# Kernel tuning notes

Hardware: AMD Instinct MI355X
Metric: run time of the kernel (lower is better)

Reference implementation:

```python
import jax, jax.numpy as jnp
import numpy as np

GAMMA = 0.9
TEMPERATURE = 0.07
BASE_TEMPERATURE = 0.07
U_SIZE = 15_000_000
BSZ, N_VIEWS, DIM = 2048, 2, 256


def setup_inputs() -> dict:
    key = jax.random.key(0)
    kf, = jax.random.split(key, 1)
    feats = jax.random.normal(kf, (BSZ, N_VIEWS, DIM), dtype=jnp.float32)
    # contrastive features are unit-normalized in practice
    feats = feats / jnp.linalg.norm(feats, axis=-1, keepdims=True)
    index = jnp.arange(BSZ, dtype=jnp.int64) if jax.config.jax_enable_x64 else jnp.arange(BSZ, dtype=jnp.int32)
    u = jnp.zeros((U_SIZE, 1), dtype=jnp.float32)
    return {"index": index, "features": feats, "u": u}


def reference(index, features, u):
    B, V, D = features.shape          # bsz, n_views, dim
    N = B * V
    eye_b = jnp.eye(B, dtype=jnp.float32)

    # torch.cat(torch.unbind(features, dim=1), dim=0) -> [V*B, D], views stacked
    contrast_feature = jnp.transpose(features, (1, 0, 2)).reshape(N, D)
    anchor_feature = contrast_feature  # contrast_mode == 'all'

    # [N, N] similarity logits
    anchor_dot_contrast = jnp.matmul(anchor_feature, contrast_feature.T) / TEMPERATURE
    logits_max = jax.lax.stop_gradient(jnp.max(anchor_dot_contrast, axis=1, keepdims=True))
    logits = anchor_dot_contrast - logits_max

    # positive mask: tiled identity with self-contrast removed
    mask = jnp.tile(eye_b, (V, V))
    logits_mask = 1.0 - jnp.eye(N, dtype=jnp.float32)  # scatter of zeros on the diagonal
    pos_mask = mask * logits_mask
    neg_mask = 1.0 - pos_mask

    # detached negative exp-logits (EMA statistics)
    neg_exp_logits = jax.lax.stop_gradient(jnp.exp(logits) * neg_mask)

    # indexed EMA buffer update: u[index] = (1-g)*u[index] + g*rowsum[:B]
    row_sum = jnp.sum(neg_exp_logits, axis=1, keepdims=True)[:B]   # [B, 1]
    u_new = (1.0 - GAMMA) * u[index] + GAMMA * row_sum             # [B, 1]
    # (buffer write: u = u.at[index].set(u_new); only u_new is read below)

    p_neg_pairs = neg_exp_logits / jnp.tile(u_new, (V, 1))         # [N, N], detached numer/denom
    log_prob = logits - jnp.sum(p_neg_pairs * logits * neg_mask, axis=1, keepdims=True)

    mean_log_prob_pos = jnp.sum(pos_mask * log_prob, axis=1) / jnp.sum(pos_mask, axis=1)
    loss = -(TEMPERATURE / BASE_TEMPERATURE) * mean_log_prob_pos
    return loss.reshape(V, B).mean()
```

## Files before the change

### kernel.cpp

```cpp
#include <hip/hip_runtime.h>


#define BSZ   2048
#define NROW  4096
#define DDIM  256
#define INVT  (1.0f / 0.07f)

typedef __attribute__((ext_vector_type(8))) __bf16 bf16x8;
typedef __attribute__((ext_vector_type(4))) float f32x4;

__device__ __forceinline__ short f2bs(float x) {
    __bf16 b = (__bf16)x;
    return __builtin_bit_cast(short, b);
}

__device__ __forceinline__ const float* crow_ptr(const float* feats, int i) {
    return feats + (((i & (BSZ - 1)) * 2 + (i >> 11)) << 8);
}

template <bool WRITE_CM>
__global__ __launch_bounds__(256) void prep_kernel(const float* __restrict__ feats,
        float* __restrict__ selfdot, float* __restrict__ EWzero,
        short* __restrict__ Cm) {
    int z = blockIdx.x * 256 + threadIdx.x;
    if (z < 2 * NROW) EWzero[z] = 0.0f;

    int lane = threadIdx.x & 63;
    int row  = (blockIdx.x << 2) + (threadIdx.x >> 6);
    const float4* src = (const float4*)crow_ptr(feats, row);
    float4 v = src[lane];
    float a0 = (float)(__bf16)v.x;
    float a1 = (float)(__bf16)v.y;
    float a2 = (float)(__bf16)v.z;
    float a3 = (float)(__bf16)v.w;
    if (WRITE_CM) {
        short4 h = make_short4(f2bs(v.x), f2bs(v.y), f2bs(v.z), f2bs(v.w));
        *(short4*)(Cm + row * DDIM + (lane << 2)) = h;
    }
    float s = a0 * a0 + a1 * a1 + a2 * a2 + a3 * a3;
    #pragma unroll
    for (int off = 32; off; off >>= 1) s += __shfl_xor(s, off, 64);
    if (lane == 0) selfdot[row] = s;
}

template <bool FROM_CM>
__device__ __forceinline__ void stage_chunk(short* lds, const float* feats,
        const short* Cm, int tileBase, int kc, int tid) {
    if (FROM_CM) {
        #pragma unroll
        for (int it = 0; it < 4; ++it) {
            int c = (it << 8) + tid;
            int r = c >> 3, c8 = c & 7;
            int4 v = *(const int4*)(Cm + (tileBase + r) * DDIM + (kc << 6) + (c8 << 3));
            *(int4*)&lds[r * 72 + (c8 << 3)] = v;
        }
    } else {
        #pragma unroll
        for (int it = 0; it < 8; ++it) {
            int c = (it << 8) + tid;
            int r = c >> 4, c4 = c & 15;
            const float4* src = (const float4*)(crow_ptr(feats, tileBase + r) + (kc << 6));
            float4 v = src[c4];
            short4 h = make_short4(f2bs(v.x), f2bs(v.y), f2bs(v.z), f2bs(v.w));
            *(short4*)&lds[r * 72 + (c4 << 2)] = h;
        }
    }
}

template <bool FROM_CM>
__global__ __launch_bounds__(256) void gemm_stats(const float* __restrict__ feats,
        const short* __restrict__ Cm, const float* __restrict__ selfdot,
        float* __restrict__ E, float* __restrict__ W, float* __restrict__ Lpos) {
    __shared__ short As[128 * 72];
    __shared__ short Bs[128 * 72];
    int tid = threadIdx.x;
    int rowBase = blockIdx.y * 128;
    int colBase = blockIdx.x * 128;

    int lane = tid & 63;
    int wave = tid >> 6;
    int quad = lane >> 4;
    int l15  = lane & 15;
    int wr = (wave >> 1) * 64;
    int wc = (wave & 1) * 64;

    f32x4 acc[4][4];
    #pragma unroll
    for (int a = 0; a < 4; ++a)
        #pragma unroll
        for (int b = 0; b < 4; ++b) acc[a][b] = (f32x4){0.f, 0.f, 0.f, 0.f};

    for (int kc = 0; kc < 4; ++kc) {
        if (kc) __syncthreads();
        stage_chunk<FROM_CM>(As, feats, Cm, rowBase, kc, tid);
        stage_chunk<FROM_CM>(Bs, feats, Cm, colBase, kc, tid);
        __syncthreads();
        #pragma unroll
        for (int kk = 0; kk < 2; ++kk) {
            int ko = (kk << 5) + (quad << 3);
            bf16x8 af[4], bfr[4];
            #pragma unroll
            for (int t = 0; t < 4; ++t)
                af[t] = *(const bf16x8*)&As[(wr + t * 16 + l15) * 72 + ko];
            #pragma unroll
            for (int t = 0; t < 4; ++t)
                bfr[t] = *(const bf16x8*)&Bs[(wc + t * 16 + l15) * 72 + ko];
            #pragma unroll
            for (int rt = 0; rt < 4; ++rt)
                #pragma unroll
                for (int ct = 0; ct < 4; ++ct)
                    acc[rt][ct] = __builtin_amdgcn_mfma_f32_16x16x32_bf16(
                        af[rt], bfr[ct], acc[rt][ct], 0, 0, 0);
        }
    }

    float sd[4][4];
    #pragma unroll
    for (int rt = 0; rt < 4; ++rt)
        #pragma unroll
        for (int r = 0; r < 4; ++r)
            sd[rt][r] = selfdot[rowBase + wr + rt * 16 + (quad << 2) + r];

    float Ep[4][4] = {}, Wp[4][4] = {};
    #pragma unroll
    for (int rt = 0; rt < 4; ++rt) {
        #pragma unroll
        for (int ct = 0; ct < 4; ++ct) {
            int gcol = colBase + wc + ct * 16 + l15;
            #pragma unroll
            for (int r = 0; r < 4; ++r) {
                int grow = rowBase + wr + rt * 16 + (quad << 2) + r;
                float l = (acc[rt][ct][r] - sd[rt][r]) * INVT;
                float e = __expf(l);
                Ep[rt][r] += e;
                Wp[rt][r] += e * l;
                if (gcol == (grow ^ BSZ)) Lpos[grow] = l;
            }
        }
    }
    #pragma unroll
    for (int rt = 0; rt < 4; ++rt) {
        #pragma unroll
        for (int r = 0; r < 4; ++r) {
            float e = Ep[rt][r], w = Wp[rt][r];
            #pragma unroll
            for (int off = 1; off < 16; off <<= 1) {
                e += __shfl_xor(e, off, 64);
                w += __shfl_xor(w, off, 64);
            }
            if (l15 == 0) {
                int grow = rowBase + wr + rt * 16 + (quad << 2) + r;
                atomicAdd(&E[grow], e);
                atomicAdd(&W[grow], w);
            }
        }
    }
}

__global__ __launch_bounds__(1024) void finalize_kernel(const int* __restrict__ index,
        const float* __restrict__ u, const float* __restrict__ E,
        const float* __restrict__ W, const float* __restrict__ Lpos,
        float* __restrict__ out) {
    __shared__ float unew[BSZ];
    __shared__ float partial[16];
    int tid = threadIdx.x;
    for (int b = tid; b < BSZ; b += 1024) {
        float lp = Lpos[b];
        float eneg = E[b] - __expf(lp);
        unew[b] = 0.1f * u[index[b]] + 0.9f * eneg;
    }
    __syncthreads();
    float local = 0.0f;
    for (int i = tid; i < NROW; i += 1024) {
        float lp  = Lpos[i];
        float elp = __expf(lp);
        float wn  = W[i] - elp * lp;
        local += lp - wn / unew[i & (BSZ - 1)];
    }
    #pragma unroll
    for (int off = 32; off; off >>= 1) local += __shfl_xor(local, off, 64);
    if ((tid & 63) == 0) partial[tid >> 6] = local;
    __syncthreads();
    if (tid == 0) {
        float s = 0.0f;
        #pragma unroll
        for (int w = 0; w < 16; ++w) s += partial[w];
        out[0] = -s / (float)NROW;
    }
}

extern "C" void kernel_launch(void* const* d_in, const int* in_sizes, int n_in,
                              void* d_out, int out_size, void* d_ws, size_t ws_size,
                              hipStream_t stream) {
    const int*   index = (const int*)d_in[0];
    const float* feats = (const float*)d_in[1];
    const float* u     = (const float*)d_in[2];
    float* out = (float*)d_out;

    float* selfdot = (float*)d_ws;
    float* E    = selfdot + NROW;
    float* W    = E + NROW;
    float* Lpos = W + NROW;
    short* Cm   = (short*)((char*)d_ws + 65536);
    bool use_cm = ws_size >= (size_t)65536 + (size_t)NROW * DDIM * 2;

    if (use_cm) {
        prep_kernel<true><<<1024, 256, 0, stream>>>(feats, selfdot, E, Cm);
        gemm_stats<true><<<dim3(32, 32), 256, 0, stream>>>(feats, Cm, selfdot, E, W, Lpos);
    } else {
        prep_kernel<false><<<1024, 256, 0, stream>>>(feats, selfdot, E, Cm);
        gemm_stats<false><<<dim3(32, 32), 256, 0, stream>>>(feats, Cm, selfdot, E, W, Lpos);
    }
    finalize_kernel<<<1, 1024, 0, stream>>>(index, u, E, W, Lpos, out);
}
```

Baseline: 128.1 us.

## Exploit Gram matrix symmetry and fuse finalize into GEMM via last-block reduction

Computes only the upper-triangular 128x128 tiles of the symmetric similarity matrix and derives column-side row statistics from each off-diagonal tile using the column self-dot shift, roughly halving MFMA work and tile loads. The separate finalize kernel is folded into the GEMM through an atomic tile counter, so the last block to finish computes the loss and one launch is saved. In exchange, off-diagonal tiles do twice the exp work in the epilogue, add more atomics, and rely on threadfence/counter ordering. The fp32 fallback path that skipped the bf16 staging buffer is dropped, so the workspace must now be large enough.

```diff
diff --git a/kernel.cpp b/kernel.cpp
--- a/kernel.cpp
+++ b/kernel.cpp
@@ -5,6 +5,8 @@
 #define NROW  4096
 #define DDIM  256
 #define INVT  (1.0f / 0.07f)
+#define NB    32
+#define NTILES (NB * (NB + 1) / 2)
 
 typedef __attribute__((ext_vector_type(8))) __bf16 bf16x8;
 typedef __attribute__((ext_vector_type(4))) float f32x4;
@@ -14,16 +16,23 @@
     return __builtin_bit_cast(short, b);
 }
 
+__device__ __forceinline__ void ag_store(float* p, float v) {
+    __hip_atomic_store(p, v, __ATOMIC_RELAXED, __HIP_MEMORY_SCOPE_AGENT);
+}
+__device__ __forceinline__ float ag_load(const float* p) {
+    return __hip_atomic_load(p, __ATOMIC_RELAXED, __HIP_MEMORY_SCOPE_AGENT);
+}
+
 __device__ __forceinline__ const float* crow_ptr(const float* feats, int i) {
     return feats + (((i & (BSZ - 1)) * 2 + (i >> 11)) << 8);
 }
 
-template <bool WRITE_CM>
 __global__ __launch_bounds__(256) void prep_kernel(const float* __restrict__ feats,
         float* __restrict__ selfdot, float* __restrict__ EWzero,
-        short* __restrict__ Cm) {
+        int* __restrict__ cnt, short* __restrict__ Cm) {
     int z = blockIdx.x * 256 + threadIdx.x;
     if (z < 2 * NROW) EWzero[z] = 0.0f;
+    if (z == 0) __hip_atomic_store(cnt, 0, __ATOMIC_RELAXED, __HIP_MEMORY_SCOPE_AGENT);
 
     int lane = threadIdx.x & 63;
     int row  = (blockIdx.x << 2) + (threadIdx.x >> 6);
@@ -33,49 +42,42 @@
     float a1 = (float)(__bf16)v.y;
     float a2 = (float)(__bf16)v.z;
     float a3 = (float)(__bf16)v.w;
-    if (WRITE_CM) {
-        short4 h = make_short4(f2bs(v.x), f2bs(v.y), f2bs(v.z), f2bs(v.w));
-        *(short4*)(Cm + row * DDIM + (lane << 2)) = h;
-    }
+    short4 h = make_short4(f2bs(v.x), f2bs(v.y), f2bs(v.z), f2bs(v.w));
+    *(short4*)(Cm + row * DDIM + (lane << 2)) = h;
     float s = a0 * a0 + a1 * a1 + a2 * a2 + a3 * a3;
     #pragma unroll
     for (int off = 32; off; off >>= 1) s += __shfl_xor(s, off, 64);
     if (lane == 0) selfdot[row] = s;
 }
 
-template <bool FROM_CM>
-__device__ __forceinline__ void stage_chunk(short* lds, const float* feats,
-        const short* Cm, int tileBase, int kc, int tid) {
-    if (FROM_CM) {
-        #pragma unroll
-        for (int it = 0; it < 4; ++it) {
-            int c = (it << 8) + tid;
-            int r = c >> 3, c8 = c & 7;
-            int4 v = *(const int4*)(Cm + (tileBase + r) * DDIM + (kc << 6) + (c8 << 3));
-            *(int4*)&lds[r * 72 + (c8 << 3)] = v;
-        }
-    } else {
-        #pragma unroll
-        for (int it = 0; it < 8; ++it) {
-            int c = (it << 8) + tid;
-            int r = c >> 4, c4 = c & 15;
-            const float4* src = (const float4*)(crow_ptr(feats, tileBase + r) + (kc << 6));
-            float4 v = src[c4];
-            short4 h = make_short4(f2bs(v.x), f2bs(v.y), f2bs(v.z), f2bs(v.w));
-            *(short4*)&lds[r * 72 + (c4 << 2)] = h;
-        }
-    }
-}
-
-template <bool FROM_CM>
-__global__ __launch_bounds__(256) void gemm_stats(const float* __restrict__ feats,
-        const short* __restrict__ Cm, const float* __restrict__ selfdot,
-        float* __restrict__ E, float* __restrict__ W, float* __restrict__ Lpos) {
+__device__ __forceinline__ void stage_chunk(short* lds, const short* Cm,
+        int tileBase, int kc, int tid) {
+    #pragma unroll
+    for (int it = 0; it < 4; ++it) {
+        int c = (it << 8) + tid;
+        int r = c >> 3, c8 = c & 7;
+        int4 v = *(const int4*)(Cm + (tileBase + r) * DDIM + (kc << 6) + (c8 << 3));
+        *(int4*)&lds[r * 72 + (c8 << 3)] = v;
+    }
+}
+
+__global__ __launch_bounds__(256) void gemm_sym(const short* __restrict__ Cm,
+        const float* __restrict__ selfdot, float* __restrict__ E,
+        float* __restrict__ W, float* __restrict__ Lpos, int* __restrict__ cnt,
+        const int* __restrict__ index, const float* __restrict__ u,
+        float* __restrict__ out) {
     __shared__ short As[128 * 72];
     __shared__ short Bs[128 * 72];
     int tid = threadIdx.x;
-    int rowBase = blockIdx.y * 128;
-    int colBase = blockIdx.x * 128;
+
+    int t = blockIdx.x;
+    int p = (int)((sqrtf(8.0f * (float)t + 1.0f) - 1.0f) * 0.5f);
+    while ((p + 1) * (p + 2) / 2 <= t) ++p;
+    while (p * (p + 1) / 2 > t) --p;
+    int q = t - p * (p + 1) / 2;
+    int rowBase = q * 128;
+    int colBase = p * 128;
+    bool offdiag = (p != q);
 
     int lane = tid & 63;
     int wave = tid >> 6;
@@ -90,21 +92,22 @@
         #pragma unroll
         for (int b = 0; b < 4; ++b) acc[a][b] = (f32x4){0.f, 0.f, 0.f, 0.f};
 
+    const short* Bsrc = offdiag ? Bs : As;
     for (int kc = 0; kc < 4; ++kc) {
         if (kc) __syncthreads();
-        stage_chunk<FROM_CM>(As, feats, Cm, rowBase, kc, tid);
-        stage_chunk<FROM_CM>(Bs, feats, Cm, colBase, kc, tid);
+        stage_chunk(As, Cm, rowBase, kc, tid);
+        if (offdiag) stage_chunk(Bs, Cm, colBase, kc, tid);
         __syncthreads();
         #pragma unroll
         for (int kk = 0; kk < 2; ++kk) {
             int ko = (kk << 5) + (quad << 3);
             bf16x8 af[4], bfr[4];
             #pragma unroll
-            for (int t = 0; t < 4; ++t)
-                af[t] = *(const bf16x8*)&As[(wr + t * 16 + l15) * 72 + ko];
-            #pragma unroll
-            for (int t = 0; t < 4; ++t)
-                bfr[t] = *(const bf16x8*)&Bs[(wc + t * 16 + l15) * 72 + ko];
+            for (int tt = 0; tt < 4; ++tt)
+                af[tt] = *(const bf16x8*)&As[(wr + tt * 16 + l15) * 72 + ko];
+            #pragma unroll
+            for (int tt = 0; tt < 4; ++tt)
+                bfr[tt] = *(const bf16x8*)&Bsrc[(wc + tt * 16 + l15) * 72 + ko];
             #pragma unroll
             for (int rt = 0; rt < 4; ++rt)
                 #pragma unroll
@@ -114,14 +117,19 @@
         }
     }
 
-    float sd[4][4];
+    float sdr[4][4];
     #pragma unroll
     for (int rt = 0; rt < 4; ++rt)
         #pragma unroll
         for (int r = 0; r < 4; ++r)
-            sd[rt][r] = selfdot[rowBase + wr + rt * 16 + (quad << 2) + r];
+            sdr[rt][r] = selfdot[rowBase + wr + rt * 16 + (quad << 2) + r];
+    float sdc[4];
+    #pragma unroll
+    for (int ct = 0; ct < 4; ++ct)
+        sdc[ct] = selfdot[colBase + wc + ct * 16 + l15];
 
     float Ep[4][4] = {}, Wp[4][4] = {};
+    float Ec[4] = {}, Wc[4] = {};
     #pragma unroll
     for (int rt = 0; rt < 4; ++rt) {
         #pragma unroll
@@ -130,11 +138,19 @@
             #pragma unroll
             for (int r = 0; r < 4; ++r) {
                 int grow = rowBase + wr + rt * 16 + (quad << 2) + r;
-                float l = (acc[rt][ct][r] - sd[rt][r]) * INVT;
+                float d = acc[rt][ct][r];
+                float l = (d - sdr[rt][r]) * INVT;
                 float e = __expf(l);
                 Ep[rt][r] += e;
                 Wp[rt][r] += e * l;
-                if (gcol == (grow ^ BSZ)) Lpos[grow] = l;
+                if (gcol == (grow ^ BSZ)) ag_store(&Lpos[grow], l);
+                if (offdiag) {
+                    float l2 = (d - sdc[ct]) * INVT;
+                    float e2 = __expf(l2);
+                    Ec[ct] += e2;
+                    Wc[ct] += e2 * l2;
+                    if (grow == (gcol ^ BSZ)) ag_store(&Lpos[gcol], l2);
+                }
             }
         }
     }
@@ -155,38 +171,46 @@
             }
         }
     }
-}
-
-__global__ __launch_bounds__(1024) void finalize_kernel(const int* __restrict__ index,
-        const float* __restrict__ u, const float* __restrict__ E,
-        const float* __restrict__ W, const float* __restrict__ Lpos,
-        float* __restrict__ out) {
-    __shared__ float unew[BSZ];
-    __shared__ float partial[16];
-    int tid = threadIdx.x;
-    for (int b = tid; b < BSZ; b += 1024) {
-        float lp = Lpos[b];
-        float eneg = E[b] - __expf(lp);
-        unew[b] = 0.1f * u[index[b]] + 0.9f * eneg;
+    if (offdiag) {
+        #pragma unroll
+        for (int ct = 0; ct < 4; ++ct) {
+            float e = Ec[ct], w = Wc[ct];
+            e += __shfl_xor(e, 16, 64);  w += __shfl_xor(w, 16, 64);
+            e += __shfl_xor(e, 32, 64);  w += __shfl_xor(w, 32, 64);
+            if (quad == 0) {
+                int gcol = colBase + wc + ct * 16 + l15;
+                atomicAdd(&E[gcol], e);
+                atomicAdd(&W[gcol], w);
+            }
+        }
+    }
+
+    __shared__ int isLast;
+    __threadfence();
+    __syncthreads();
+    if (tid == 0) isLast = (atomicAdd(cnt, 1) == NTILES - 1);
+    __syncthreads();
+    if (!isLast) return;
+    __threadfence();
+
+    float* unew = (float*)As;
+    for (int b = tid; b < BSZ; b += 256) {
+        float lp = ag_load(&Lpos[b]);
+        unew[b] = 0.1f * u[index[b]] + 0.9f * (ag_load(&E[b]) - __expf(lp));
     }
     __syncthreads();
     float local = 0.0f;
-    for (int i = tid; i < NROW; i += 1024) {
-        float lp  = Lpos[i];
+    for (int i = tid; i < NROW; i += 256) {
+        float lp  = ag_load(&Lpos[i]);
         float elp = __expf(lp);
-        float wn  = W[i] - elp * lp;
-        local += lp - wn / unew[i & (BSZ - 1)];
+        local += lp - (ag_load(&W[i]) - elp * lp) / unew[i & (BSZ - 1)];
     }
     #pragma unroll
     for (int off = 32; off; off >>= 1) local += __shfl_xor(local, off, 64);
-    if ((tid & 63) == 0) partial[tid >> 6] = local;
-    __syncthreads();
-    if (tid == 0) {
-        float s = 0.0f;
-        #pragma unroll
-        for (int w = 0; w < 16; ++w) s += partial[w];
-        out[0] = -s / (float)NROW;
-    }
+    __shared__ float part[4];
+    if (lane == 0) part[wave] = local;
+    __syncthreads();
+    if (tid == 0) out[0] = -(part[0] + part[1] + part[2] + part[3]) / (float)NROW;
 }
 
 extern "C" void kernel_launch(void* const* d_in, const int* in_sizes, int n_in,
@@ -201,15 +225,9 @@
     float* E    = selfdot + NROW;
     float* W    = E + NROW;
     float* Lpos = W + NROW;
-    short* Cm   = (short*)((char*)d_ws + 65536);
-    bool use_cm = ws_size >= (size_t)65536 + (size_t)NROW * DDIM * 2;
-
-    if (use_cm) {
-        prep_kernel<true><<<1024, 256, 0, stream>>>(feats, selfdot, E, Cm);
-        gemm_stats<true><<<dim3(32, 32), 256, 0, stream>>>(feats, Cm, selfdot, E, W, Lpos);
-    } else {
-        prep_kernel<false><<<1024, 256, 0, stream>>>(feats, selfdot, E, Cm);
-        gemm_stats<false><<<dim3(32, 32), 256, 0, stream>>>(feats, Cm, selfdot, E, W, Lpos);
-    }
-    finalize_kernel<<<1, 1024, 0, stream>>>(index, u, E, W, Lpos, out);
-}
+    int*   cnt  = (int*)(Lpos + NROW);
+    short* Cm   = (short*)((char*)d_ws + 131072);
+
+    prep_kernel<<<1024, 256, 0, stream>>>(feats, selfdot, E, cnt, Cm);
+    gemm_sym<<<NTILES, 256, 0, stream>>>(Cm, selfdot, E, W, Lpos, cnt, index, u, out);
+}
```

Result: slower. 149.7 us (+16.9%).
